# Optimization experiments

Hardware: AMD Instinct MI355X
Metric: run time of the kernel (lower is better)

## Reference

```python
import jax, jax.numpy as jnp
import numpy as np

EPS = 1e-5

@jax.custom_vjp
def binarize(x):
    # sign binarization used by Conv2d_1w1a (1-bit weights and activations)
    return jnp.where(x >= 0, 1.0, -1.0).astype(x.dtype)

def _bin_fwd(x):
    return binarize(x), x

def _bin_bwd(x, g):
    # straight-through estimator with hardtanh clipping (standard BNN STE)
    return (g * (jnp.abs(x) <= 1.0).astype(g.dtype),)

binarize.defvjp(_bin_fwd, _bin_bwd)

def setup_inputs() -> dict:
    key = jax.random.key(0)
    k1, k2, k3 = jax.random.split(key, 3)
    B, C_in, H, W = 32, 256, 56, 56
    C_half = 512 // 2
    x = jax.random.normal(k1, (B, C_in, H, W), dtype=jnp.float32)
    gamma = jnp.ones((C_in,), dtype=jnp.float32)
    beta = jnp.zeros((C_in,), dtype=jnp.float32)
    w1 = jax.random.normal(k2, (C_half, C_in), dtype=jnp.float32) * 0.05
    w2 = jax.random.normal(k3, (C_half, C_in), dtype=jnp.float32) * 0.05
    return {"x": x, "gamma": gamma, "beta": beta, "w1": w1, "w2": w2}

def reference(x, gamma, beta, w1, w2):
    # BatchNorm2d (training mode: batch statistics, biased variance)
    mean = jnp.mean(x, axis=(0, 2, 3), keepdims=True)
    var = jnp.var(x, axis=(0, 2, 3), keepdims=True)
    xn = (x - mean) * jax.lax.rsqrt(var + EPS)
    xn = xn * gamma[None, :, None, None] + beta[None, :, None, None]

    # binarize activations once; both convs consume the same binarized map
    a = binarize(xn)
    b1 = binarize(w1)  # [C_half, C_in]
    b2 = binarize(w2)

    # 1x1 stride-2 conv == strided slice + channel contraction
    a1 = a[:, :, ::2, ::2]      # conv_1 path
    a2 = a[:, :, 1::2, 1::2]    # conv_2 path on out[:, :, 1:, 1:]

    out1 = jnp.einsum('bchw,oc->bohw', a1, b1)
    out2 = jnp.einsum('bchw,oc->bohw', a2, b2)
    return jnp.concatenate([out1, out2], axis=1)
```

## Files before the change

### kernel.cpp

```cpp
#include <hip/hip_runtime.h>
#include <stdint.h>

#define CIN 256
#define HW4 784
#define NB  32
#define NHO 28
#define NWO 28

__global__ __launch_bounds__(256) void k_stage1(const float* __restrict__ x,
                          const float* __restrict__ w1, const float* __restrict__ w2,
                          double* __restrict__ part, unsigned long long* __restrict__ wp) {
    int blk = blockIdx.x;
    int tid = threadIdx.x;
    if (blk < 2048) {
        int c = blk >> 3, chunk = blk & 7;
        double s = 0.0, sq = 0.0;
        for (int bq = 0; bq < 4; ++bq) {
            int b = chunk * 4 + bq;
            const float4* base = (const float4*)x + (size_t)(b * CIN + c) * HW4;
            for (int i = tid; i < HW4; i += 256) {
                float4 v = base[i];
                double a0 = v.x, a1 = v.y, a2 = v.z, a3 = v.w;
                s  += (a0 + a1) + (a2 + a3);
                sq += (a0*a0 + a1*a1) + (a2*a2 + a3*a3);
            }
        }
        __shared__ double ls[256], lq[256];
        ls[tid] = s; lq[tid] = sq;
        __syncthreads();
        for (int off = 128; off > 0; off >>= 1) {
            if (tid < off) { ls[tid] += ls[tid+off]; lq[tid] += lq[tid+off]; }
            __syncthreads();
        }
        if (tid == 0) {
            part[(chunk*256 + c)*2]   = ls[0];
            part[(chunk*256 + c)*2+1] = lq[0];
        }
    } else {
        int wave = tid >> 6, l = tid & 63;
        int baseTask = ((blk - 2048)*4 + wave)*4;
        #pragma unroll
        for (int t = 0; t < 4; ++t) {
            int w_idx = baseTask + t;
            int p = w_idx >> 10, rem = w_idx & 1023;
            int o = rem >> 2, wv = rem & 3;
            const float* w = p ? w2 : w1;
            float v = w[o*256 + wv*64 + l];
            unsigned long long m = __ballot(v >= 0.0f);
            if (l == 0) wp[w_idx] = m;
        }
    }
}

__global__ __launch_bounds__(256) void k_fused(const float* __restrict__ x,
    const double* __restrict__ part, const float* __restrict__ gamma,
    const float* __restrict__ beta, const unsigned long long* __restrict__ wp,
    float* __restrict__ out) {
    __shared__ double sm[256], ssg[256], sbt[256];
    __shared__ unsigned char pred[256*60];
    __shared__ unsigned long long wl[2048];
    __shared__ unsigned long long apl[224];
    int blk = blockIdx.x;
    int b = blk / NHO, ho = blk % NHO;
    int tid = threadIdx.x;

    {
        const ulonglong2* src = (const ulonglong2*)wp;
        ulonglong2* dst = (ulonglong2*)wl;
        for (int k = tid; k < 1024; k += 256) dst[k] = src[k];
    }
    {
        int c = tid;
        double s = 0.0, sq = 0.0;
        for (int k = 0; k < 8; ++k) {
            s  += part[(k*256 + c)*2];
            sq += part[(k*256 + c)*2+1];
        }
        const double n = 100352.0;
        double mean = s / n;
        double var  = sq / n - mean*mean;
        if (var < 0.0) var = 0.0;
        double invstd = 1.0 / sqrt(var + 1e-5);
        sm[c] = mean; ssg[c] = invstd * (double)gamma[c]; sbt[c] = (double)beta[c];
    }
    __syncthreads();

    #pragma unroll 4
    for (int k = 0; k < 28; ++k) {
        int i4 = tid + k*256;
        int c = i4 / 28, r4 = i4 - c*28;
        float4 v = ((const float4*)x)[(size_t)(b*CIN + c)*HW4 + ho*28 + r4];
        double m = sm[c], sg = ssg[c], bt = sbt[c];
        unsigned short bits; int off;
        if (r4 < 14) {
            bits  = (((double)v.x - m)*sg + bt >= 0.0) ? 1u : 0u;
            bits |= (((double)v.z - m)*sg + bt >= 0.0) ? 0x100u : 0u;
            off = c*60 + 2*r4;
        } else {
            bits  = (((double)v.y - m)*sg + bt >= 0.0) ? 1u : 0u;
            bits |= (((double)v.w - m)*sg + bt >= 0.0) ? 0x100u : 0u;
            off = c*60 + 28 + 2*(r4 - 14);
        }
        *(unsigned short*)&pred[off] = bits;
    }
    __syncthreads();

    {
        int g = tid >> 6, l = tid & 63;
        int c = g*64 + l;
        for (int p = 0; p < 2; ++p)
            for (int wo = 0; wo < NWO; ++wo) {
                unsigned char pr = pred[c*60 + p*28 + wo];
                unsigned long long mask = __ballot(pr != 0);
                if (l == 0) apl[p*112 + wo*4 + g] = mask;
            }
    }
    __syncthreads();

    int o_sub = tid >> 5, wi = tid & 31;
    if (wi >= NWO) return;
    unsigned long long a0[2][4];
    for (int p = 0; p < 2; ++p)
        #pragma unroll
        for (int j = 0; j < 4; ++j) a0[p][j] = apl[p*112 + wi*4 + j];
    for (int p = 0; p < 2; ++p) {
        size_t outbase = ((size_t)(b*512 + p*256))*784 + (size_t)ho*NWO + wi;
        #pragma unroll 4
        for (int og = 0; og < 32; ++og) {
            int o = og*8 + o_sub;
            const unsigned long long* w = &wl[p*1024 + o*4];
            int d = __popcll(a0[p][0]^w[0]) + __popcll(a0[p][1]^w[1])
                  + __popcll(a0[p][2]^w[2]) + __popcll(a0[p][3]^w[3]);
            out[outbase + (size_t)o*784] = (float)(256 - 2*d);
        }
    }
}

extern "C" void kernel_launch(void* const* d_in, const int* in_sizes, int n_in,
                              void* d_out, int out_size, void* d_ws, size_t ws_size,
                              hipStream_t stream) {
    const float* x     = (const float*)d_in[0];
    const float* gamma = (const float*)d_in[1];
    const float* beta  = (const float*)d_in[2];
    const float* w1    = (const float*)d_in[3];
    const float* w2    = (const float*)d_in[4];
    float* out = (float*)d_out;

    char* ws = (char*)d_ws;
    double* part = (double*)ws;
    unsigned long long* wp = (unsigned long long*)(ws + 40960);

    k_stage1<<<2176, 256, 0, stream>>>(x, w1, w2, part, wp);
    k_fused<<<NB*NHO, 256, 0, stream>>>(x, part, gamma, beta, wp, out);
}
```

Before: 206.0 us.

## Read packed weights from global with wave-uniform indices instead of LDS copy

Interleaves the packed weight bitmasks per output channel (both convs adjacent) and drops the 16KB LDS staging copy in the fused kernel. The popcount stage is remapped so each wave handles one conv path and half the output channels, with wave-uniform weight addresses (readfirstlane) that can become scalar loads. The binarize branch is also made branchless. This cuts LDS use and should allow higher occupancy, but lanes 28-63 of each wave sit idle and each wave's loop runs longer.

Result: slower. 210.6 us (+2.3%).

```diff
diff --git a/kernel.cpp b/kernel.cpp
--- a/kernel.cpp
+++ b/kernel.cpp
@@ -9,7 +9,7 @@
 
 __global__ __launch_bounds__(256) void k_stage1(const float* __restrict__ x,
                           const float* __restrict__ w1, const float* __restrict__ w2,
-                          double* __restrict__ part, unsigned long long* __restrict__ wp) {
+                          double* __restrict__ part, unsigned long long* __restrict__ wq) {
     int blk = blockIdx.x;
     int tid = threadIdx.x;
     if (blk < 2048) {
@@ -42,33 +42,26 @@
         #pragma unroll
         for (int t = 0; t < 4; ++t) {
             int w_idx = baseTask + t;
-            int p = w_idx >> 10, rem = w_idx & 1023;
-            int o = rem >> 2, wv = rem & 3;
+            int o = w_idx >> 3, p = (w_idx >> 2) & 1, wv = w_idx & 3;
             const float* w = p ? w2 : w1;
             float v = w[o*256 + wv*64 + l];
             unsigned long long m = __ballot(v >= 0.0f);
-            if (l == 0) wp[w_idx] = m;
+            if (l == 0) wq[w_idx] = m;
         }
     }
 }
 
 __global__ __launch_bounds__(256) void k_fused(const float* __restrict__ x,
     const double* __restrict__ part, const float* __restrict__ gamma,
-    const float* __restrict__ beta, const unsigned long long* __restrict__ wp,
+    const float* __restrict__ beta, const unsigned long long* __restrict__ wq,
     float* __restrict__ out) {
     __shared__ double sm[256], ssg[256], sbt[256];
     __shared__ unsigned char pred[256*60];
-    __shared__ unsigned long long wl[2048];
     __shared__ unsigned long long apl[224];
     int blk = blockIdx.x;
     int b = blk / NHO, ho = blk % NHO;
     int tid = threadIdx.x;
 
-    {
-        const ulonglong2* src = (const ulonglong2*)wp;
-        ulonglong2* dst = (ulonglong2*)wl;
-        for (int k = tid; k < 1024; k += 256) dst[k] = src[k];
-    }
     {
         int c = tid;
         double s = 0.0, sq = 0.0;
@@ -91,16 +84,13 @@
         int c = i4 / 28, r4 = i4 - c*28;
         float4 v = ((const float4*)x)[(size_t)(b*CIN + c)*HW4 + ho*28 + r4];
         double m = sm[c], sg = ssg[c], bt = sbt[c];
-        unsigned short bits; int off;
-        if (r4 < 14) {
-            bits  = (((double)v.x - m)*sg + bt >= 0.0) ? 1u : 0u;
-            bits |= (((double)v.z - m)*sg + bt >= 0.0) ? 0x100u : 0u;
-            off = c*60 + 2*r4;
-        } else {
-            bits  = (((double)v.y - m)*sg + bt >= 0.0) ? 1u : 0u;
-            bits |= (((double)v.w - m)*sg + bt >= 0.0) ? 0x100u : 0u;
-            off = c*60 + 28 + 2*(r4 - 14);
-        }
+        bool e = (r4 < 14);
+        float f0 = e ? v.x : v.y;
+        float f1 = e ? v.z : v.w;
+        int off = c*60 + (e ? 2*r4 : 28 + 2*(r4 - 14));
+        unsigned short bits;
+        bits  = (((double)f0 - m)*sg + bt >= 0.0) ? 1u : 0u;
+        bits |= (((double)f1 - m)*sg + bt >= 0.0) ? 0x100u : 0u;
         *(unsigned short*)&pred[off] = bits;
     }
     __syncthreads();
@@ -117,21 +107,23 @@
     }
     __syncthreads();
 
-    int o_sub = tid >> 5, wi = tid & 31;
-    if (wi >= NWO) return;
-    unsigned long long a0[2][4];
-    for (int p = 0; p < 2; ++p)
-        #pragma unroll
-        for (int j = 0; j < 4; ++j) a0[p][j] = apl[p*112 + wi*4 + j];
-    for (int p = 0; p < 2; ++p) {
-        size_t outbase = ((size_t)(b*512 + p*256))*784 + (size_t)ho*NWO + wi;
-        #pragma unroll 4
-        for (int og = 0; og < 32; ++og) {
-            int o = og*8 + o_sub;
-            const unsigned long long* w = &wl[p*1024 + o*4];
-            int d = __popcll(a0[p][0]^w[0]) + __popcll(a0[p][1]^w[1])
-                  + __popcll(a0[p][2]^w[2]) + __popcll(a0[p][3]^w[3]);
-            out[outbase + (size_t)o*784] = (float)(256 - 2*d);
+    {
+        int wid = __builtin_amdgcn_readfirstlane(tid >> 6);
+        int p = wid >> 1, sub = wid & 1;
+        int wi = tid & 63;
+        if (wi < NWO) {
+            unsigned long long a0[4];
+            #pragma unroll
+            for (int j = 0; j < 4; ++j) a0[j] = apl[p*112 + wi*4 + j];
+            size_t outb = ((size_t)(b*512 + p*256))*784 + (size_t)ho*NWO + wi;
+            #pragma unroll 4
+            for (int og = 0; og < 128; ++og) {
+                int o = og*2 + sub;
+                const unsigned long long* wr = wq + o*8 + p*4;
+                int d = __popcll(a0[0]^wr[0]) + __popcll(a0[1]^wr[1])
+                      + __popcll(a0[2]^wr[2]) + __popcll(a0[3]^wr[3]);
+                out[outb + (size_t)o*784] = (float)(256 - 2*d);
+            }
         }
     }
 }
@@ -148,8 +140,8 @@
 
     char* ws = (char*)d_ws;
     double* part = (double*)ws;
-    unsigned long long* wp = (unsigned long long*)(ws + 40960);
+    unsigned long long* wq = (unsigned long long*)(ws + 40960);
 
-    k_stage1<<<2176, 256, 0, stream>>>(x, w1, w2, part, wp);
-    k_fused<<<NB*NHO, 256, 0, stream>>>(x, part, gamma, beta, wp, out);
+    k_stage1<<<2176, 256, 0, stream>>>(x, w1, w2, part, wq);
+    k_fused<<<NB*NHO, 256, 0, stream>>>(x, part, gamma, beta, wq, out);
 }
```
